# Kernel tuning notes

Measured on AMD Instinct MI355X. Metric: run time of the kernel, lower is better.

Reference implementation:

```python
import jax, jax.numpy as jnp
import numpy as np

TEMPERATURE = 0.5


def setup_inputs() -> dict:
    key = jax.random.key(0)
    k1, k2 = jax.random.split(key)
    emb_i = jax.random.normal(k1, (4096, 512), dtype=jnp.float32)
    emb_j = jax.random.normal(k2, (4096, 512), dtype=jnp.float32)
    return {"emb_i": emb_i, "emb_j": emb_j}


def reference(emb_i, emb_j):
    # NT-Xent (SimCLR) loss, vectorized over the original per-sample python loop.
    N = emb_i.shape[0]
    z_i = emb_i / jnp.linalg.norm(emb_i, axis=1, keepdims=True)
    z_j = emb_j / jnp.linalg.norm(emb_j, axis=1, keepdims=True)
    z = jnp.concatenate([z_i, z_j], axis=0)  # [2N, d]
    # cosine similarity of unit vectors == dot product
    sim = z @ z.T                             # [2N, 2N]
    exp_sim = jnp.exp(sim / TEMPERATURE)
    # denominator excludes self-similarity (the scatter-zero in the original)
    denom = exp_sim.sum(axis=1) - jnp.diagonal(exp_sim)
    idx = jnp.arange(2 * N)
    pos_idx = jnp.concatenate([jnp.arange(N) + N, jnp.arange(N)])
    num = exp_sim[idx, pos_idx]               # positive-pair similarities
    loss = -jnp.log(num / denom)
    return loss.mean()
```

## Files before the change

### kernel.cpp

```cpp
#include <hip/hip_runtime.h>
#include <hip/hip_bf16.h>

typedef __attribute__((ext_vector_type(4))) int i32x4;

#define AS1 __attribute__((address_space(1)))
#define AS3 __attribute__((address_space(3)))

#define DDIM 512
#define BK 64

__global__ __launch_bounds__(256) void norm_pd_kernel(
    const float* __restrict__ ei, const float* __restrict__ ej,
    unsigned char* __restrict__ zq, float* __restrict__ pd,
    float* __restrict__ rowsum, float* __restrict__ out, int N) {
  const int k = blockIdx.x;
  const int t = threadIdx.x;
  const float2 a = *reinterpret_cast<const float2*>(ei + (size_t)k * DDIM + t * 2);
  const float2 b = *reinterpret_cast<const float2*>(ej + (size_t)k * DDIM + t * 2);
  float sii = a.x * a.x + a.y * a.y;
  float sjj = b.x * b.x + b.y * b.y;
  float sij = a.x * b.x + a.y * b.y;
#pragma unroll
  for (int off = 32; off; off >>= 1) {
    sii += __shfl_down(sii, off);
    sjj += __shfl_down(sjj, off);
    sij += __shfl_down(sij, off);
  }
  __shared__ float red[3][4];
  if ((t & 63) == 0) { red[0][t >> 6] = sii; red[1][t >> 6] = sjj; red[2][t >> 6] = sij; }
  __syncthreads();
  sii = red[0][0] + red[0][1] + red[0][2] + red[0][3];
  sjj = red[1][0] + red[1][1] + red[1][2] + red[1][3];
  sij = red[2][0] + red[2][1] + red[2][2] + red[2][3];
  const float rsi = rsqrtf(sii), rsj = rsqrtf(sjj);

  const int qa0 = (int)rintf(127.0f * a.x * rsi);
  const int qa1 = (int)rintf(127.0f * a.y * rsi);
  const int qb0 = (int)rintf(127.0f * b.x * rsj);
  const int qb1 = (int)rintf(127.0f * b.y * rsj);
  const unsigned short wa = (unsigned short)(qa0 & 0xff) | ((unsigned short)(qa1 & 0xff) << 8);
  const unsigned short wb = (unsigned short)(qb0 & 0xff) | ((unsigned short)(qb1 & 0xff) << 8);
  *reinterpret_cast<unsigned short*>(zq + (size_t)k * DDIM + t * 2) = wa;
  *reinterpret_cast<unsigned short*>(zq + (size_t)(N + k) * DDIM + t * 2) = wb;
  if (t == 0) {
    pd[k] = sij * rsi * rsj;
    rowsum[k] = 0.0f;
    rowsum[N + k] = 0.0f;
    if (k == 0) out[0] = 0.0f;
  }
}


#define MFMAI8(A, B, C) __builtin_amdgcn_mfma_i32_16x16x64_i8((A), (B), (C), 0, 0, 0)

__global__ __launch_bounds__(256, 4) void simloss_main(
    const unsigned char* __restrict__ zq, float* __restrict__ rowsum, int nwg) {
  const int orig = blockIdx.x;
  const int q = nwg >> 3, r8 = nwg & 7;
  const int xcd = orig & 7, pos0 = orig >> 3;
  const int t0 = (xcd < r8 ? xcd * (q + 1) : r8 * (q + 1) + (xcd - r8) * q) + pos0;

  const float ff = sqrtf(8.0f * (float)t0 + 1.0f);
  int by = (int)((ff - 1.0f) * 0.5f);
  while ((by + 1) * (by + 2) / 2 <= t0) ++by;
  while (by * (by + 1) / 2 > t0) --by;
  const int bx = t0 - by * (by + 1) / 2;

  const int row0 = bx * 128;
  const int col0 = by * 128;

  __shared__ unsigned char lds[3][2][8192];

  const int tid = threadIdx.x;
  const int w = tid >> 6;
  const int l = tid & 63;
  const int wr = (w >> 1) * 64;
  const int wc = (w & 1) * 64;
  const int lrow = l & 15;
  const int g = l >> 4;

  i32x4 acc[4][4] = {};

  auto stage = [&](int buf, int k0) {
#pragma unroll
    for (int half = 0; half < 2; ++half) {
      const int baserow = half ? col0 : row0;
#pragma unroll
      for (int it = 0; it < 2; ++it) {
        const int pp = it * 256 + tid;
        const int row = pp >> 2;
        const int s = pp & 3;
        const int gs = (s - (row >> 1)) & 3;
        const unsigned char* src = zq + (size_t)(baserow + row) * DDIM + k0 + gs * 16;
        char* dst = (char*)&lds[buf][half][0] + (unsigned)((it * 256 + w * 64) * 16);
        __builtin_amdgcn_global_load_lds((const AS1 void*)src, (AS3 void*)dst, 16, 0, 0);
      }
    }
  };

  auto compute = [&](int buf) {
    const unsigned char* ab = &lds[buf][0][0];
    const unsigned char* bb = &lds[buf][1][0];
    i32x4 Af[4], Bf[4];
#pragma unroll
    for (int mf = 0; mf < 4; ++mf) {
      const int rr = wr + mf * 16 + lrow;
      Af[mf] = *reinterpret_cast<const i32x4*>(ab + rr * 64 + (((g + (rr >> 1)) & 3) << 4));
    }
#pragma unroll
    for (int nf = 0; nf < 4; ++nf) {
      const int cc = wc + nf * 16 + lrow;
      Bf[nf] = *reinterpret_cast<const i32x4*>(bb + cc * 64 + (((g + (cc >> 1)) & 3) << 4));
    }
#pragma unroll
    for (int mf = 0; mf < 4; ++mf)
#pragma unroll
      for (int nf = 0; nf < 4; ++nf)
        acc[mf][nf] = MFMAI8(Af[mf], Bf[nf], acc[mf][nf]);
  };

  stage(0, 0);
  stage(1, BK);

#pragma unroll
  for (int t = 0; t < 8; ++t) {
    if (t < 6) {
      stage((t + 2) % 3, (t + 2) * BK);
      asm volatile("s_waitcnt vmcnt(8)" ::: "memory");
    } else if (t == 6) {
      asm volatile("s_waitcnt vmcnt(4)" ::: "memory");
    } else {
      asm volatile("s_waitcnt vmcnt(0)" ::: "memory");
    }
    __builtin_amdgcn_s_barrier();
    compute(t % 3);
    __builtin_amdgcn_s_barrier();
  }

  const float SC = 2.0f * 1.44269504088896340736f / 16129.0f;
  const int lgrp = l >> 4;
  const int lcol = l & 15;

  float e[4][4][4];
#pragma unroll
  for (int mf = 0; mf < 4; ++mf)
#pragma unroll
    for (int nf = 0; nf < 4; ++nf)
#pragma unroll
      for (int rg = 0; rg < 4; ++rg)
        e[mf][nf][rg] = exp2f((float)acc[mf][nf][rg] * SC);

#pragma unroll
  for (int mf = 0; mf < 4; ++mf) {
    float rs[4];
#pragma unroll
    for (int rg = 0; rg < 4; ++rg) {
      float s = 0.0f;
#pragma unroll
      for (int nf = 0; nf < 4; ++nf) s += e[mf][nf][rg];
      rs[rg] = s;
    }
#pragma unroll
    for (int off = 1; off < 16; off <<= 1) {
#pragma unroll
      for (int rg = 0; rg < 4; ++rg) rs[rg] += __shfl_xor(rs[rg], off);
    }
    if (lcol == 0) {
      const int rowb = row0 + wr + mf * 16 + lgrp * 4;
#pragma unroll
      for (int rg = 0; rg < 4; ++rg) atomicAdd(&rowsum[rowb + rg], rs[rg]);
    }
  }

  if (bx != by) {
#pragma unroll
    for (int nf = 0; nf < 4; ++nf) {
      float cs = 0.0f;
#pragma unroll
      for (int mf = 0; mf < 4; ++mf)
#pragma unroll
        for (int rg = 0; rg < 4; ++rg) cs += e[mf][nf][rg];
      cs += __shfl_xor(cs, 16);
      cs += __shfl_xor(cs, 32);
      if (lgrp == 0) atomicAdd(&rowsum[col0 + wc + nf * 16 + lcol], cs);
    }
  }
}

__global__ __launch_bounds__(1024) void finalize_kernel(
    const float* __restrict__ rowsum, const float* __restrict__ pd,
    float* __restrict__ out, int M, int N) {
  const int i = blockIdx.x * 1024 + threadIdx.x;
  const float E2 = 7.38905609893065f;
  float acc = 0.0f;
  if (i < M) {
    const float denom = rowsum[i] - E2;
    const int kk = (i < N) ? i : (i - N);
    acc = logf(denom) - 2.0f * pd[kk];
  }
#pragma unroll
  for (int off = 32; off; off >>= 1) acc += __shfl_down(acc, off);
  __shared__ float red[16];
  const int t = threadIdx.x;
  if ((t & 63) == 0) red[t >> 6] = acc;
  __syncthreads();
  if (t < 64) {
    float s = (t < 16) ? red[t] : 0.0f;
#pragma unroll
    for (int off = 8; off; off >>= 1) s += __shfl_down(s, off);
    if (t == 0) atomicAdd(out, s / (float)M);
  }
}

extern "C" void kernel_launch(void* const* d_in, const int* in_sizes, int n_in,
                              void* d_out, int out_size, void* d_ws, size_t ws_size,
                              hipStream_t stream) {
  const float* ei = (const float*)d_in[0];
  const float* ej = (const float*)d_in[1];
  float* out = (float*)d_out;

  const int N = in_sizes[0] / DDIM;
  const int M = 2 * N;
  const int NT = M / 128;
  const int NTRI = NT * (NT + 1) / 2;

  char* ws = (char*)d_ws;
  unsigned char* zq = (unsigned char*)ws;
  float* pd = (float*)(ws + (size_t)M * DDIM);
  float* rowsum = (float*)(ws + (size_t)M * DDIM + (size_t)N * 4);

  norm_pd_kernel<<<N, 256, 0, stream>>>(ei, ej, zq, pd, rowsum, out, N);
  simloss_main<<<NTRI, 256, 0, stream>>>(zq, rowsum, NTRI);
  finalize_kernel<<<(M + 1023) / 1024, 1024, 0, stream>>>(rowsum, pd, out, M, N);
}
```

Before: 47.48 us.

## Use one wave per row in normalize kernel and double-buffer GEMM LDS

The normalize/quantize kernel now assigns one 64-lane wavefront per row, using float4 loads, a wave-only xor reduction with no shared memory or block barrier, and 8-byte packed int8 stores. It launches a quarter as many blocks. Separately, the int8 MFMA similarity kernel goes from a 3-stage to a 2-stage LDS pipeline, which cuts LDS from 48KB to 32KB per block to allow more resident blocks. The cost is a shallower prefetch, so less load latency is hidden per block.

```diff
diff --git a/kernel.cpp b/kernel.cpp
--- a/kernel.cpp
+++ b/kernel.cpp
@@ -13,36 +13,41 @@
     const float* __restrict__ ei, const float* __restrict__ ej,
     unsigned char* __restrict__ zq, float* __restrict__ pd,
     float* __restrict__ rowsum, float* __restrict__ out, int N) {
-  const int k = blockIdx.x;
-  const int t = threadIdx.x;
-  const float2 a = *reinterpret_cast<const float2*>(ei + (size_t)k * DDIM + t * 2);
-  const float2 b = *reinterpret_cast<const float2*>(ej + (size_t)k * DDIM + t * 2);
-  float sii = a.x * a.x + a.y * a.y;
-  float sjj = b.x * b.x + b.y * b.y;
-  float sij = a.x * b.x + a.y * b.y;
+  const int k = blockIdx.x * 4 + (threadIdx.x >> 6);
+  const int l = threadIdx.x & 63;
+
+  const float4 a0 = *reinterpret_cast<const float4*>(ei + (size_t)k * DDIM + l * 8);
+  const float4 a1 = *reinterpret_cast<const float4*>(ei + (size_t)k * DDIM + l * 8 + 4);
+  const float4 b0 = *reinterpret_cast<const float4*>(ej + (size_t)k * DDIM + l * 8);
+  const float4 b1 = *reinterpret_cast<const float4*>(ej + (size_t)k * DDIM + l * 8 + 4);
+
+  float sii = a0.x*a0.x + a0.y*a0.y + a0.z*a0.z + a0.w*a0.w
+            + a1.x*a1.x + a1.y*a1.y + a1.z*a1.z + a1.w*a1.w;
+  float sjj = b0.x*b0.x + b0.y*b0.y + b0.z*b0.z + b0.w*b0.w
+            + b1.x*b1.x + b1.y*b1.y + b1.z*b1.z + b1.w*b1.w;
+  float sij = a0.x*b0.x + a0.y*b0.y + a0.z*b0.z + a0.w*b0.w
+            + a1.x*b1.x + a1.y*b1.y + a1.z*b1.z + a1.w*b1.w;
 #pragma unroll
   for (int off = 32; off; off >>= 1) {
-    sii += __shfl_down(sii, off);
-    sjj += __shfl_down(sjj, off);
-    sij += __shfl_down(sij, off);
-  }
-  __shared__ float red[3][4];
-  if ((t & 63) == 0) { red[0][t >> 6] = sii; red[1][t >> 6] = sjj; red[2][t >> 6] = sij; }
-  __syncthreads();
-  sii = red[0][0] + red[0][1] + red[0][2] + red[0][3];
-  sjj = red[1][0] + red[1][1] + red[1][2] + red[1][3];
-  sij = red[2][0] + red[2][1] + red[2][2] + red[2][3];
+    sii += __shfl_xor(sii, off);
+    sjj += __shfl_xor(sjj, off);
+    sij += __shfl_xor(sij, off);
+  }
   const float rsi = rsqrtf(sii), rsj = rsqrtf(sjj);
 
-  const int qa0 = (int)rintf(127.0f * a.x * rsi);
-  const int qa1 = (int)rintf(127.0f * a.y * rsi);
-  const int qb0 = (int)rintf(127.0f * b.x * rsj);
-  const int qb1 = (int)rintf(127.0f * b.y * rsj);
-  const unsigned short wa = (unsigned short)(qa0 & 0xff) | ((unsigned short)(qa1 & 0xff) << 8);
-  const unsigned short wb = (unsigned short)(qb0 & 0xff) | ((unsigned short)(qb1 & 0xff) << 8);
-  *reinterpret_cast<unsigned short*>(zq + (size_t)k * DDIM + t * 2) = wa;
-  *reinterpret_cast<unsigned short*>(zq + (size_t)(N + k) * DDIM + t * 2) = wb;
-  if (t == 0) {
+  unsigned char qa[8], qb[8];
+  const float av[8] = {a0.x, a0.y, a0.z, a0.w, a1.x, a1.y, a1.z, a1.w};
+  const float bv[8] = {b0.x, b0.y, b0.z, b0.w, b1.x, b1.y, b1.z, b1.w};
+#pragma unroll
+  for (int i = 0; i < 8; ++i) {
+    qa[i] = (unsigned char)((int)rintf(127.0f * av[i] * rsi) & 0xff);
+    qb[i] = (unsigned char)((int)rintf(127.0f * bv[i] * rsj) & 0xff);
+  }
+  *reinterpret_cast<uint2*>(zq + (size_t)k * DDIM + l * 8) =
+      *reinterpret_cast<const uint2*>(qa);
+  *reinterpret_cast<uint2*>(zq + (size_t)(N + k) * DDIM + l * 8) =
+      *reinterpret_cast<const uint2*>(qb);
+  if (l == 0) {
     pd[k] = sij * rsi * rsj;
     rowsum[k] = 0.0f;
     rowsum[N + k] = 0.0f;
@@ -69,7 +74,7 @@
   const int row0 = bx * 128;
   const int col0 = by * 128;
 
-  __shared__ unsigned char lds[3][2][8192];
+  __shared__ unsigned char lds[2][2][8192];
 
   const int tid = threadIdx.x;
   const int w = tid >> 6;
@@ -120,22 +125,19 @@
   };
 
   stage(0, 0);
-  stage(1, BK);
-
-#pragma unroll
-  for (int t = 0; t < 8; ++t) {
-    if (t < 6) {
-      stage((t + 2) % 3, (t + 2) * BK);
-      asm volatile("s_waitcnt vmcnt(8)" ::: "memory");
-    } else if (t == 6) {
-      asm volatile("s_waitcnt vmcnt(4)" ::: "memory");
-    } else {
-      asm volatile("s_waitcnt vmcnt(0)" ::: "memory");
-    }
+
+#pragma unroll
+  for (int t = 0; t < 7; ++t) {
+    const int buf = t & 1;
+    stage(buf ^ 1, (t + 1) * BK);
+    asm volatile("s_waitcnt vmcnt(4)" ::: "memory");
     __builtin_amdgcn_s_barrier();
-    compute(t % 3);
+    compute(buf);
     __builtin_amdgcn_s_barrier();
   }
+  asm volatile("s_waitcnt vmcnt(0)" ::: "memory");
+  __builtin_amdgcn_s_barrier();
+  compute(1);
 
   const float SC = 2.0f * 1.44269504088896340736f / 16129.0f;
   const int lgrp = l >> 4;
@@ -229,7 +231,7 @@
   float* pd = (float*)(ws + (size_t)M * DDIM);
   float* rowsum = (float*)(ws + (size_t)M * DDIM + (size_t)N * 4);
 
-  norm_pd_kernel<<<N, 256, 0, stream>>>(ei, ej, zq, pd, rowsum, out, N);
+  norm_pd_kernel<<<N / 4, 256, 0, stream>>>(ei, ej, zq, pd, rowsum, out, N);
   simloss_main<<<NTRI, 256, 0, stream>>>(zq, rowsum, NTRI);
   finalize_kernel<<<(M + 1023) / 1024, 1024, 0, stream>>>(rowsum, pd, out, M, N);
 }
```

Measured after the change: 44.43 us (median of 2 runs). -6.4%, faster.
